# Kernel tuning notes

Measured on AMD Instinct MI355X. Metric: run time of the kernel, lower is better.

Reference implementation:

```python
import jax, jax.numpy as jnp
import numpy as np

# --- Instant-NGP hashgrid config (from INGP.build_encoding) ---
L = 16            # cfg_model.encoding.levels
F = 2             # cfg_model.encoding.hashgrid.dim
T = 1 << 19       # 2 ** log2_hashmap_size
BASE = 16         # 2 ** min_logres
FINEST = 2048     # 2 ** max_logres
GROWTH = np.exp((np.log(FINEST) - np.log(BASE)) / (L - 1))
RES = np.floor(BASE * GROWTH ** np.arange(L)).astype(np.float32)  # per-level resolution
VMIN, VMAX = -1.0, 1.0  # voxel_range
N_POINTS = 524288

# 8 trilinear corner offsets, and NGP spatial-hash primes
CORNERS = np.array([[i, j, k] for i in (0, 1) for j in (0, 1) for k in (0, 1)],
                   dtype=np.uint32)                       # [8,3]
PRIMES = np.array([1, 2654435761, 805459861], dtype=np.uint32)


def setup_inputs() -> dict:
    key = jax.random.key(0)
    k1, k2 = jax.random.split(key)
    points_3D = jax.random.uniform(k1, (N_POINTS, 3), minval=-1.0, maxval=1.0,
                                   dtype=jnp.float32)
    # torch-ngp 'uniform' init: U(-1e-4, 1e-4)
    tables = jax.random.uniform(k2, (L, T, F), minval=-1e-4, maxval=1e-4,
                                dtype=jnp.float32)
    return {"points_3D": points_3D, "tables": tables}


def _hash_encode(x, tables):
    """x: [N,3] in [0,1]; tables: [L,T,F] -> [N, L*F]."""
    corners_u = jnp.asarray(CORNERS)            # [8,3] uint32
    corners_b = jnp.asarray(CORNERS.astype(bool))
    p0u, p1u, p2u = (jnp.uint32(int(p)) for p in PRIMES)
    mask = jnp.uint32(T - 1)

    def level(table, r):
        pos = x * r                              # [N,3]
        p0 = jnp.floor(pos)
        w = pos - p0                             # trilinear weights [N,3]
        c = p0.astype(jnp.uint32)[:, None, :] + corners_u[None]  # [N,8,3]
        h = (c[..., 0] * p0u) ^ (c[..., 1] * p1u) ^ (c[..., 2] * p2u)
        idx = (h & mask).astype(jnp.int32)       # [N,8] hashed bucket ids
        vals = table[idx]                        # [N,8,F] irregular gather
        wc = jnp.where(corners_b[None], w[:, None, :], 1.0 - w[:, None, :]).prod(-1)
        return jnp.einsum('nc,ncf->nf', wc, vals)  # [N,F]

    feats = jax.vmap(level)(tables, jnp.asarray(RES))  # [L,N,F]
    n = x.shape[0]
    return jnp.transpose(feats, (1, 0, 2)).reshape(n, L * F)


def reference(points_3D, tables):
    # _encode_3D with contract=False: normalize to [0,1] over voxel_range
    x = (points_3D - VMIN) / (VMAX - VMIN)
    feat = _hash_encode(x, tables)
    return feat.astype(jnp.float32)
```

## Files before the change

### kernel.cpp

```cpp
#include <hip/hip_runtime.h>
#include <cmath>


constexpr int LVLS = 16;
constexpr unsigned TBL = 1u << 19;
constexpr unsigned TMASK = TBL - 1u;
constexpr unsigned P1 = 2654435761u;
constexpr unsigned P2 = 805459861u;
constexpr int PTS_PER_BLOCK = 512;

typedef float vf2 __attribute__((ext_vector_type(2)));
typedef float vf4 __attribute__((ext_vector_type(4)));

struct ResArr { float r[LVLS]; };

template<bool USE_WS>
__global__ __launch_bounds__(256) void ingp_gather(
    const float* __restrict__ pts,
    const float* __restrict__ tables,
    float2* __restrict__ dst,
    ResArr ra, int npts, int bpl)
{
    __shared__ float s_res[LVLS];
    if (threadIdx.x < LVLS) s_res[threadIdx.x] = ra.r[threadIdx.x];
    __syncthreads();

    int b = blockIdx.x;
    int phase_blocks = 8 * bpl;
    int xcd = b & 7;
    int phase = b / phase_blocks;
    int lvl = phase == 0 ? xcd : 15 - xcd;
    int q = (b % phase_blocks) >> 3;
    int t = threadIdx.x;

    float r = s_res[lvl];
    const float2* __restrict__ tab = (const float2*)tables + (size_t)lvl * TBL;

    int p[2];
    p[0] = q * PTS_PER_BLOCK + t;
    p[1] = p[0] + 256;

    #pragma unroll
    for (int s = 0; s < 2; ++s) {
        bool valid = p[s] < npts;
        int pp = valid ? p[s] : 0;
        float px = __builtin_nontemporal_load(pts + pp * 3 + 0);
        float py = __builtin_nontemporal_load(pts + pp * 3 + 1);
        float pz = __builtin_nontemporal_load(pts + pp * 3 + 2);
        float x = (px + 1.0f) * 0.5f;
        float y = (py + 1.0f) * 0.5f;
        float z = (pz + 1.0f) * 0.5f;
        float posx = x * r, posy = y * r, posz = z * r;
        float fx = floorf(posx), fy = floorf(posy), fz = floorf(posz);
        float wx = posx - fx, wy = posy - fy, wz = posz - fz;
        unsigned ix = (unsigned)fx, iy = (unsigned)fy, iz = (unsigned)fz;
        unsigned hx0 = ix,      hx1 = ix + 1u;
        unsigned hy0 = iy * P1, hy1 = hy0 + P1;
        unsigned hz0 = iz * P2, hz1 = hz0 + P2;

        unsigned hyz[4];
        hyz[0] = hy0 ^ hz0;
        hyz[1] = hy0 ^ hz1;
        hyz[2] = hy1 ^ hz0;
        hyz[3] = hy1 ^ hz1;

        float2 v[8];
        if ((ix & 1u) == 0u) {
            #pragma unroll
            for (int yz = 0; yz < 4; ++yz) {
                unsigned b0 = (hx0 ^ hyz[yz]) & TMASK;
                const vf4* lp = (const vf4*)(tab + (b0 & ~1u));
                vf4 qd = *lp;
                float2 lo = make_float2(qd.x, qd.y);
                float2 hi = make_float2(qd.z, qd.w);
                bool odd = (b0 & 1u) != 0u;
                v[yz]     = odd ? hi : lo;
                v[4 + yz] = odd ? lo : hi;
            }
        } else {
            #pragma unroll
            for (int yz = 0; yz < 4; ++yz) {
                unsigned b0 = (hx0 ^ hyz[yz]) & TMASK;
                unsigned b1 = (hx1 ^ hyz[yz]) & TMASK;
                v[yz]     = tab[b0];
                v[4 + yz] = tab[b1];
            }
        }

        float ox = 1.0f - wx, oy = 1.0f - wy, oz = 1.0f - wz;
        float w[8];
        w[0] = (ox * oy) * oz;
        w[1] = (ox * oy) * wz;
        w[2] = (ox * wy) * oz;
        w[3] = (ox * wy) * wz;
        w[4] = (wx * oy) * oz;
        w[5] = (wx * oy) * wz;
        w[6] = (wx * wy) * oz;
        w[7] = (wx * wy) * wz;

        float f0 = w[0] * v[0].x;
        float f1 = w[0] * v[0].y;
        #pragma unroll
        for (int c = 1; c < 8; ++c) {
            f0 += w[c] * v[c].x;
            f1 += w[c] * v[c].y;
        }
        if (valid) {
            vf2 o; o.x = f0; o.y = f1;
            if (USE_WS)
                __builtin_nontemporal_store(o, (vf2*)(dst + (size_t)lvl * npts + p[s]));
            else
                dst[(size_t)p[s] * LVLS + lvl] = make_float2(f0, f1);
        }
    }
}

__global__ __launch_bounds__(256) void ingp_transpose(
    const float2* __restrict__ ws, float4* __restrict__ out, int npts)
{
    __shared__ float2 a[LVLS][258];
    int base = blockIdx.x * 256;
    int t = threadIdx.x;

    #pragma unroll
    for (int l = 0; l < LVLS; ++l) {
        int pp = base + t;
        float2 val = make_float2(0.f, 0.f);
        if (pp < npts) {
            vf2 v = __builtin_nontemporal_load((const vf2*)(ws + (size_t)l * npts + pp));
            val = make_float2(v.x, v.y);
        }
        a[l][t] = val;
    }
    __syncthreads();

    int j = t & 7;
    int pl = t >> 3;
    #pragma unroll
    for (int it = 0; it < 8; ++it) {
        int pt = pl + it * 32;
        if (base + pt < npts) {
            float2 u = a[2 * j][pt];
            float2 v = a[2 * j + 1][pt];
            vf4 o; o.x = u.x; o.y = u.y; o.z = v.x; o.w = v.y;
            __builtin_nontemporal_store(o, (vf4*)(out + (size_t)(base + pt) * 8 + j));
        }
    }
}

extern "C" void kernel_launch(void* const* d_in, const int* in_sizes, int n_in,
                              void* d_out, int out_size, void* d_ws, size_t ws_size,
                              hipStream_t stream) {
    const float* pts    = (const float*)d_in[0];
    const float* tables = (const float*)d_in[1];
    int npts = in_sizes[0] / 3;

    ResArr ra;
    double growth = exp((log(2048.0) - log(16.0)) / 15.0);
    for (int l = 0; l < LVLS; ++l)
        ra.r[l] = (float)floor(16.0 * pow(growth, (double)l));

    int bpl = (npts + PTS_PER_BLOCK - 1) / PTS_PER_BLOCK;
    int grid = LVLS * bpl;

    size_t ws_needed = (size_t)LVLS * npts * sizeof(float2);
    bool use_ws = ws_size >= ws_needed;

    if (use_ws) {
        float2* ws = (float2*)d_ws;
        hipLaunchKernelGGL(ingp_gather<true>, dim3(grid), dim3(256), 0, stream,
                           pts, tables, ws, ra, npts, bpl);
        hipLaunchKernelGGL(ingp_transpose, dim3((npts + 255) / 256), dim3(256), 0, stream,
                           ws, (float4*)d_out, npts);
    } else {
        hipLaunchKernelGGL(ingp_gather<false>, dim3(grid), dim3(256), 0, stream,
                           pts, tables, (float2*)d_out, ra, npts, bpl);
    }
}
```

Baseline: 314.1 us.

## Fuse per-level gather and transpose into one pass over all levels per point

Replaces the two-kernel scheme (per-level gather into a level-major workspace, then a transpose kernel) with a single kernel where each thread loops over all 16 levels for its two points, keeps results in registers, and transposes through shared memory before coalesced stores. This removes the workspace write and read round trip and the second launch. In exchange it drops the XCD-aware level-to-block mapping, so every block gathers from all 16 tables, which may hurt L2 locality. It also raises register pressure with 64 accumulators per thread under a launch bound of 4 blocks.

```diff
diff --git a/kernel.cpp b/kernel.cpp
--- a/kernel.cpp
+++ b/kernel.cpp
@@ -7,143 +7,126 @@
 constexpr unsigned TMASK = TBL - 1u;
 constexpr unsigned P1 = 2654435761u;
 constexpr unsigned P2 = 805459861u;
-constexpr int PTS_PER_BLOCK = 512;
 
-typedef float vf2 __attribute__((ext_vector_type(2)));
 typedef float vf4 __attribute__((ext_vector_type(4)));
 
 struct ResArr { float r[LVLS]; };
 
-template<bool USE_WS>
-__global__ __launch_bounds__(256) void ingp_gather(
+__global__ __launch_bounds__(256, 4) void ingp_onepass(
     const float* __restrict__ pts,
     const float* __restrict__ tables,
-    float2* __restrict__ dst,
-    ResArr ra, int npts, int bpl)
+    float* __restrict__ out,
+    ResArr ra, int npts)
 {
-    __shared__ float s_res[LVLS];
-    if (threadIdx.x < LVLS) s_res[threadIdx.x] = ra.r[threadIdx.x];
-    __syncthreads();
+    int t = threadIdx.x;
+    int base = blockIdx.x * 512;
 
-    int b = blockIdx.x;
-    int phase_blocks = 8 * bpl;
-    int xcd = b & 7;
-    int phase = b / phase_blocks;
-    int lvl = phase == 0 ? xcd : 15 - xcd;
-    int q = (b % phase_blocks) >> 3;
-    int t = threadIdx.x;
-
-    float r = s_res[lvl];
-    const float2* __restrict__ tab = (const float2*)tables + (size_t)lvl * TBL;
-
-    int p[2];
-    p[0] = q * PTS_PER_BLOCK + t;
-    p[1] = p[0] + 256;
-
+    float X[2], Y[2], Z[2];
+    bool valid[2];
+    int pidx[2] = { base + t, base + t + 256 };
     #pragma unroll
     for (int s = 0; s < 2; ++s) {
-        bool valid = p[s] < npts;
-        int pp = valid ? p[s] : 0;
+        valid[s] = pidx[s] < npts;
+        int pp = valid[s] ? pidx[s] : 0;
         float px = __builtin_nontemporal_load(pts + pp * 3 + 0);
         float py = __builtin_nontemporal_load(pts + pp * 3 + 1);
         float pz = __builtin_nontemporal_load(pts + pp * 3 + 2);
-        float x = (px + 1.0f) * 0.5f;
-        float y = (py + 1.0f) * 0.5f;
-        float z = (pz + 1.0f) * 0.5f;
-        float posx = x * r, posy = y * r, posz = z * r;
-        float fx = floorf(posx), fy = floorf(posy), fz = floorf(posz);
-        float wx = posx - fx, wy = posy - fy, wz = posz - fz;
-        unsigned ix = (unsigned)fx, iy = (unsigned)fy, iz = (unsigned)fz;
-        unsigned hx0 = ix,      hx1 = ix + 1u;
-        unsigned hy0 = iy * P1, hy1 = hy0 + P1;
-        unsigned hz0 = iz * P2, hz1 = hz0 + P2;
+        X[s] = (px + 1.0f) * 0.5f;
+        Y[s] = (py + 1.0f) * 0.5f;
+        Z[s] = (pz + 1.0f) * 0.5f;
+    }
 
-        unsigned hyz[4];
-        hyz[0] = hy0 ^ hz0;
-        hyz[1] = hy0 ^ hz1;
-        hyz[2] = hy1 ^ hz0;
-        hyz[3] = hy1 ^ hz1;
-
-        float2 v[8];
-        if ((ix & 1u) == 0u) {
-            #pragma unroll
-            for (int yz = 0; yz < 4; ++yz) {
-                unsigned b0 = (hx0 ^ hyz[yz]) & TMASK;
-                const vf4* lp = (const vf4*)(tab + (b0 & ~1u));
-                vf4 qd = *lp;
-                float2 lo = make_float2(qd.x, qd.y);
-                float2 hi = make_float2(qd.z, qd.w);
-                bool odd = (b0 & 1u) != 0u;
-                v[yz]     = odd ? hi : lo;
-                v[4 + yz] = odd ? lo : hi;
-            }
-        } else {
-            #pragma unroll
-            for (int yz = 0; yz < 4; ++yz) {
-                unsigned b0 = (hx0 ^ hyz[yz]) & TMASK;
-                unsigned b1 = (hx1 ^ hyz[yz]) & TMASK;
-                v[yz]     = tab[b0];
-                v[4 + yz] = tab[b1];
-            }
-        }
-
-        float ox = 1.0f - wx, oy = 1.0f - wy, oz = 1.0f - wz;
-        float w[8];
-        w[0] = (ox * oy) * oz;
-        w[1] = (ox * oy) * wz;
-        w[2] = (ox * wy) * oz;
-        w[3] = (ox * wy) * wz;
-        w[4] = (wx * oy) * oz;
-        w[5] = (wx * oy) * wz;
-        w[6] = (wx * wy) * oz;
-        w[7] = (wx * wy) * wz;
-
-        float f0 = w[0] * v[0].x;
-        float f1 = w[0] * v[0].y;
-        #pragma unroll
-        for (int c = 1; c < 8; ++c) {
-            f0 += w[c] * v[c].x;
-            f1 += w[c] * v[c].y;
-        }
-        if (valid) {
-            vf2 o; o.x = f0; o.y = f1;
-            if (USE_WS)
-                __builtin_nontemporal_store(o, (vf2*)(dst + (size_t)lvl * npts + p[s]));
-            else
-                dst[(size_t)p[s] * LVLS + lvl] = make_float2(f0, f1);
-        }
-    }
-}
-
-__global__ __launch_bounds__(256) void ingp_transpose(
-    const float2* __restrict__ ws, float4* __restrict__ out, int npts)
-{
-    __shared__ float2 a[LVLS][258];
-    int base = blockIdx.x * 256;
-    int t = threadIdx.x;
+    float acc[2][LVLS][2];
 
     #pragma unroll
     for (int l = 0; l < LVLS; ++l) {
-        int pp = base + t;
-        float2 val = make_float2(0.f, 0.f);
-        if (pp < npts) {
-            vf2 v = __builtin_nontemporal_load((const vf2*)(ws + (size_t)l * npts + pp));
-            val = make_float2(v.x, v.y);
+        float r = ra.r[l];
+        const float2* __restrict__ tab = (const float2*)tables + (size_t)l * TBL;
+
+        #pragma unroll
+        for (int s = 0; s < 2; ++s) {
+            float posx = X[s] * r, posy = Y[s] * r, posz = Z[s] * r;
+            float fx = floorf(posx), fy = floorf(posy), fz = floorf(posz);
+            float wx = posx - fx, wy = posy - fy, wz = posz - fz;
+            unsigned ix = (unsigned)fx, iy = (unsigned)fy, iz = (unsigned)fz;
+            unsigned hx0 = ix,      hx1 = ix + 1u;
+            unsigned hy0 = iy * P1, hy1 = hy0 + P1;
+            unsigned hz0 = iz * P2, hz1 = hz0 + P2;
+
+            unsigned hyz[4];
+            hyz[0] = hy0 ^ hz0;
+            hyz[1] = hy0 ^ hz1;
+            hyz[2] = hy1 ^ hz0;
+            hyz[3] = hy1 ^ hz1;
+
+            float2 v[8];
+            if ((ix & 1u) == 0u) {
+                #pragma unroll
+                for (int yz = 0; yz < 4; ++yz) {
+                    unsigned b0 = (hx0 ^ hyz[yz]) & TMASK;
+                    const vf4* lp = (const vf4*)(tab + (b0 & ~1u));
+                    vf4 qd = *lp;
+                    float2 lo = make_float2(qd.x, qd.y);
+                    float2 hi = make_float2(qd.z, qd.w);
+                    bool odd = (b0 & 1u) != 0u;
+                    v[yz]     = odd ? hi : lo;
+                    v[4 + yz] = odd ? lo : hi;
+                }
+            } else {
+                #pragma unroll
+                for (int yz = 0; yz < 4; ++yz) {
+                    unsigned b0 = (hx0 ^ hyz[yz]) & TMASK;
+                    unsigned b1 = (hx1 ^ hyz[yz]) & TMASK;
+                    v[yz]     = tab[b0];
+                    v[4 + yz] = tab[b1];
+                }
+            }
+
+            float ox = 1.0f - wx, oy = 1.0f - wy, oz = 1.0f - wz;
+            float w[8];
+            w[0] = (ox * oy) * oz;
+            w[1] = (ox * oy) * wz;
+            w[2] = (ox * wy) * oz;
+            w[3] = (ox * wy) * wz;
+            w[4] = (wx * oy) * oz;
+            w[5] = (wx * oy) * wz;
+            w[6] = (wx * wy) * oz;
+            w[7] = (wx * wy) * wz;
+
+            float f0 = w[0] * v[0].x;
+            float f1 = w[0] * v[0].y;
+            #pragma unroll
+            for (int c = 1; c < 8; ++c) {
+                f0 += w[c] * v[c].x;
+                f1 += w[c] * v[c].y;
+            }
+            acc[s][l][0] = f0;
+            acc[s][l][1] = f1;
         }
-        a[l][t] = val;
     }
-    __syncthreads();
 
+    __shared__ float2 lds[256][17];
     int j = t & 7;
-    int pl = t >> 3;
+    int pr = t >> 3;
+
     #pragma unroll
-    for (int it = 0; it < 8; ++it) {
-        int pt = pl + it * 32;
-        if (base + pt < npts) {
-            float2 u = a[2 * j][pt];
-            float2 v = a[2 * j + 1][pt];
-            vf4 o; o.x = u.x; o.y = u.y; o.z = v.x; o.w = v.y;
-            __builtin_nontemporal_store(o, (vf4*)(out + (size_t)(base + pt) * 8 + j));
+    for (int h = 0; h < 2; ++h) {
+        if (h) __syncthreads();
+        #pragma unroll
+        for (int l = 0; l < LVLS; ++l)
+            lds[t][l] = make_float2(acc[h][l][0], acc[h][l][1]);
+        __syncthreads();
+
+        #pragma unroll
+        for (int it = 0; it < 8; ++it) {
+            int pt = pr + it * 32;
+            int gp = base + h * 256 + pt;
+            if (gp < npts) {
+                float2 u = lds[pt][2 * j];
+                float2 w2 = lds[pt][2 * j + 1];
+                vf4 o; o.x = u.x; o.y = u.y; o.z = w2.x; o.w = w2.y;
+                __builtin_nontemporal_store(o, (vf4*)(out + (size_t)gp * 32 + j * 4));
+            }
         }
     }
 }
@@ -160,20 +143,7 @@
     for (int l = 0; l < LVLS; ++l)
         ra.r[l] = (float)floor(16.0 * pow(growth, (double)l));
 
-    int bpl = (npts + PTS_PER_BLOCK - 1) / PTS_PER_BLOCK;
-    int grid = LVLS * bpl;
-
-    size_t ws_needed = (size_t)LVLS * npts * sizeof(float2);
-    bool use_ws = ws_size >= ws_needed;
-
-    if (use_ws) {
-        float2* ws = (float2*)d_ws;
-        hipLaunchKernelGGL(ingp_gather<true>, dim3(grid), dim3(256), 0, stream,
-                           pts, tables, ws, ra, npts, bpl);
-        hipLaunchKernelGGL(ingp_transpose, dim3((npts + 255) / 256), dim3(256), 0, stream,
-                           ws, (float4*)d_out, npts);
-    } else {
-        hipLaunchKernelGGL(ingp_gather<false>, dim3(grid), dim3(256), 0, stream,
-                           pts, tables, (float2*)d_out, ra, npts, bpl);
-    }
+    int grid = (npts + 511) / 512;
+    hipLaunchKernelGGL(ingp_onepass, dim3(grid), dim3(256), 0, stream,
+                       pts, tables, (float*)d_out, ra, npts);
 }
```

After: 813.9 us. 2.59x slower.
